# Performance work log

Measured on AMD Instinct MI355X. Metric: run time of the kernel, lower is better.

Reference implementation:

```python
import jax, jax.numpy as jnp
import numpy as np

D_MODEL = 768
D_HIDDEN = 2048
N_HEADS = 12
D_HEAD = 64
REG_COEFF = 1e-3
EPS = 1e-6
BATCH = 4
SEQ = 128


def setup_inputs() -> dict:
    key = jax.random.key(0)
    ks = jax.random.split(key, 4)
    # kaiming_uniform_ on (fan_in, fan_out)-shaped tensors: bound = sqrt(6 / fan_in_torch)
    # (values only need to be plausible; exact init dist is irrelevant for the kernel baseline)
    s_enc = 1.0 / np.sqrt(D_MODEL)
    s_dec = 1.0 / np.sqrt(D_HIDDEN)
    return {
        "x": jax.random.normal(ks[0], (BATCH, SEQ, D_MODEL), dtype=jnp.float32),
        "W_encQ": jax.random.normal(ks[1], (D_MODEL, D_HIDDEN), dtype=jnp.float32) * s_enc,
        "W_encK": jax.random.normal(ks[2], (D_MODEL, D_HIDDEN), dtype=jnp.float32) * s_enc,
        "b_encQ": jnp.zeros((D_HIDDEN,), dtype=jnp.float32),
        "b_encK": jnp.zeros((D_HIDDEN,), dtype=jnp.float32),
        "W_dec": jax.random.normal(ks[3], (D_HIDDEN, N_HEADS), dtype=jnp.float32) * s_dec,
        "b_dec": jnp.zeros((N_HEADS,), dtype=jnp.float32),
    }


def reference(x, W_encQ, W_encK, b_encQ, b_encK, W_dec, b_dec):
    # queries/keys: (batch, posn, d_hidden)
    queries = jax.nn.relu(jnp.einsum("bsd,dh->bsh", x, W_encQ) + b_encQ)
    keys = jax.nn.relu(jnp.einsum("bsd,dh->bsh", x, W_encK) + b_encK)
    # acts: (batch, posn_q, posn_k, d_hidden) -- the huge multi-use intermediate
    acts = queries[:, :, None, :] * keys[:, None, :, :]
    reg_loss = REG_COEFF * jnp.sum(jnp.sqrt(jnp.abs(acts) + EPS))
    feature_fires = (acts > 0).astype(jnp.int32)
    # decode to per-head scores: (batch, posn_q, posn_k, n_heads)
    score = jnp.einsum("bqkh,hn->bqkn", acts, W_dec) / np.sqrt(D_HEAD) + b_dec
    score = jnp.transpose(score, (0, 3, 1, 2))  # (batch, n_heads, posn_q, posn_k)
    return score, reg_loss, feature_fires
```

## Files before the change

### kernel.cpp

```cpp
#include <hip/hip_runtime.h>
#include <hip/hip_bf16.h>

#define D_MODEL 768
#define D_HIDDEN 2048
#define NHEADS 12
#define BATCH 4
#define SEQ 128
#define MROWS (BATCH*SEQ)
#define SCORE_ELEMS (BATCH*NHEADS*SEQ*SEQ)
#define REG_OFF SCORE_ELEMS
#define FIRES_OFF (SCORE_ELEMS + 1)
#define NROWS_T 65536
#define FIRES_WAVES 2048
#define FIRES_BLOCKS 512
#define SCORE_BLOCKS (BATCH*NHEADS*16)
#define TRIGCAP 64

typedef __attribute__((ext_vector_type(8))) short bf16x8;
typedef __attribute__((ext_vector_type(4))) float f32x4;

static __device__ __forceinline__ unsigned short f2bf(float f) {
    union { float f; unsigned u; } v; v.f = f;
    unsigned u = v.u;
    return (unsigned short)((u + 0x7FFFu + ((u >> 16) & 1u)) >> 16);
}

static __device__ __forceinline__ void split_bf16(float v, short& hi, short& lo) {
    unsigned short h = f2bf(v);
    float hf = __uint_as_float((unsigned)h << 16);
    float lf = v - hf;
    hi = (short)h;
    lo = (short)f2bf(lf);
}

static __device__ __forceinline__ float fsqrt_fast(float x) {
    return __builtin_amdgcn_sqrtf(x);
}

__global__ __launch_bounds__(256) void enc_kernel(
    const float* __restrict__ x,
    const float* __restrict__ WQ, const float* __restrict__ WK,
    const float* __restrict__ bQ, const float* __restrict__ bK,
    float* __restrict__ qbuf, float* __restrict__ kbuf,
    float* __restrict__ out)
{
    __shared__ unsigned tcnt;
    __shared__ unsigned tlist[TRIGCAP];
    __shared__ double   redd[4];

    const int bufid = blockIdx.z;
    const float* W    = bufid ? WK : WQ;
    const float* bias = bufid ? bK : bQ;
    float* outbuf     = bufid ? kbuf : qbuf;

    const int t  = threadIdx.x;
    if (t == 0) tcnt = 0u;
    if (blockIdx.x == 0 && blockIdx.y == 0 && blockIdx.z == 0 && t == 0)
        out[REG_OFF] = 0.f;
    __syncthreads();

    const int w  = t >> 6;
    const int l  = t & 63;
    const int mt = blockIdx.y * 64 + (w >> 1) * 32;
    const int nt = blockIdx.x * 64 + (w & 1) * 32;
    const int lr = l & 15;
    const int hg = (l >> 4) * 8;

    f32x4 acc[2][2];
    #pragma unroll
    for (int i = 0; i < 2; ++i)
        #pragma unroll
        for (int j = 0; j < 2; ++j) { f32x4 z = {0.f, 0.f, 0.f, 0.f}; acc[i][j] = z; }

    for (int kk = 0; kk < D_MODEL; kk += 32) {
        const int h0 = kk + hg;
        bf16x8 ah[2], al[2], bh[2], bl[2];
        #pragma unroll
        for (int fi = 0; fi < 2; ++fi) {
            const float* xp = x + (size_t)(mt + fi * 16 + lr) * D_MODEL + h0;
            const float4 v1 = *reinterpret_cast<const float4*>(xp);
            const float4 v2 = *reinterpret_cast<const float4*>(xp + 4);
            const float vv[8] = {v1.x, v1.y, v1.z, v1.w, v2.x, v2.y, v2.z, v2.w};
            #pragma unroll
            for (int i = 0; i < 8; ++i) {
                short h_, lo_;
                split_bf16(vv[i], h_, lo_);
                ah[fi][i] = h_; al[fi][i] = lo_;
            }
        }
        #pragma unroll
        for (int fj = 0; fj < 2; ++fj) {
            const int col = nt + fj * 16 + lr;
            #pragma unroll
            for (int i = 0; i < 8; ++i) {
                short h_, lo_;
                split_bf16(W[(size_t)(h0 + i) * D_HIDDEN + col], h_, lo_);
                bh[fj][i] = h_; bl[fj][i] = lo_;
            }
        }
        #pragma unroll
        for (int fi = 0; fi < 2; ++fi)
            #pragma unroll
            for (int fj = 0; fj < 2; ++fj) {
                acc[fi][fj] = __builtin_amdgcn_mfma_f32_16x16x32_bf16(
                    ah[fi], bh[fj], acc[fi][fj], 0, 0, 0);
                acc[fi][fj] = __builtin_amdgcn_mfma_f32_16x16x32_bf16(
                    ah[fi], bl[fj], acc[fi][fj], 0, 0, 0);
                acc[fi][fj] = __builtin_amdgcn_mfma_f32_16x16x32_bf16(
                    al[fi], bh[fj], acc[fi][fj], 0, 0, 0);
            }
    }

    #pragma unroll
    for (int fi = 0; fi < 2; ++fi)
        #pragma unroll
        for (int fj = 0; fj < 2; ++fj)
            #pragma unroll
            for (int j = 0; j < 4; ++j) {
                const int row = mt + fi * 16 + (l >> 4) * 4 + j;
                const int col = nt + fj * 16 + lr;
                float pre = acc[fi][fj][j] + bias[col];
                if (fabsf(pre) < 3e-4f) {
                    unsigned idx = atomicAdd(&tcnt, 1u);
                    if (idx < TRIGCAP) {
                        tlist[idx] = ((unsigned)row << 11) | (unsigned)col;
                    } else {
                        const float* xr = x + (size_t)row * D_MODEL;
                        const float* wc = W + col;
                        double s = (double)bias[col];
                        for (int dd = 0; dd < D_MODEL; ++dd)
                            s += (double)xr[dd] * (double)wc[(size_t)dd * D_HIDDEN];
                        pre = (float)s;
                    }
                }
                outbuf[(size_t)row * D_HIDDEN + col] = fmaxf(pre, 0.f);
            }

    __syncthreads();
    const unsigned n = min(tcnt, (unsigned)TRIGCAP);
    for (unsigned i = 0; i < n; ++i) {
        const unsigned e = tlist[i];
        const int hh = (int)(e & 2047u);
        const int mm = (int)(e >> 11);
        double s = 0.0;
        #pragma unroll
        for (int k = 0; k < 3; ++k) {
            const int dd = t + k * 256;
            s += (double)x[(size_t)mm * D_MODEL + dd]
               * (double)W[(size_t)dd * D_HIDDEN + hh];
        }
        #pragma unroll
        for (int off = 32; off > 0; off >>= 1) s += __shfl_down(s, off);
        if (l == 0) redd[w] = s;
        __syncthreads();
        if (t == 0) {
            double tot = redd[0] + redd[1] + redd[2] + redd[3] + (double)bias[hh];
            outbuf[(size_t)mm * D_HIDDEN + hh] = fmaxf((float)tot, 0.f);
        }
        __syncthreads();
    }
}

__global__ __launch_bounds__(256) void main_kernel(
    const float* __restrict__ qbuf, const float* __restrict__ kbuf,
    const float* __restrict__ Wdec, const float* __restrict__ bdec,
    float* __restrict__ out)
{
    __shared__ float wcol[D_HIDDEN];
    __shared__ float red[4][64][16];
    __shared__ float rs[4];
    const int t  = threadIdx.x;
    const int bi = blockIdx.x;

    if (bi < SCORE_BLOCKS) {
        const int sub = bi & 15;
        const int pr  = bi >> 4;
        const int n   = pr % NHEADS;
        const int b   = pr / NHEADS;

        for (int idx = t; idx < D_HIDDEN; idx += 256)
            wcol[idx] = Wdec[(size_t)idx * NHEADS + n];
        __syncthreads();

        const int qt   = (sub >> 2) * 32;
        const int kt   = (sub & 3) * 32;
        const int w    = t >> 6;
        const int lane = t & 63;
        const int lrow = lane & 15;
        const int koff = (lane >> 4) * 8;

        f32x4 acc[2][2];
        #pragma unroll
        for (int i = 0; i < 2; ++i)
            #pragma unroll
            for (int j = 0; j < 2; ++j) { f32x4 z = {0.f, 0.f, 0.f, 0.f}; acc[i][j] = z; }

        const float* qb = qbuf + (size_t)b * SEQ * D_HIDDEN;
        const float* kb = kbuf + (size_t)b * SEQ * D_HIDDEN;

        const int hlo = w * 512;
        for (int kk = hlo; kk < hlo + 512; kk += 32) {
            const int h0 = kk + koff;
            float wv[8];
            #pragma unroll
            for (int i = 0; i < 8; ++i) wv[i] = wcol[h0 + i];

            bf16x8 afrag[2], bfrag[2];
            #pragma unroll
            for (int fi = 0; fi < 2; ++fi) {
                const float* qp = qb + (size_t)(qt + fi * 16 + lrow) * D_HIDDEN + h0;
                const float4 q1 = *reinterpret_cast<const float4*>(qp);
                const float4 q2 = *reinterpret_cast<const float4*>(qp + 4);
                const float qf[8] = {q1.x, q1.y, q1.z, q1.w, q2.x, q2.y, q2.z, q2.w};
                #pragma unroll
                for (int i = 0; i < 8; ++i) afrag[fi][i] = (short)f2bf(qf[i] * wv[i]);
            }
            #pragma unroll
            for (int fj = 0; fj < 2; ++fj) {
                const float* kp = kb + (size_t)(kt + fj * 16 + lrow) * D_HIDDEN + h0;
                const float4 k1 = *reinterpret_cast<const float4*>(kp);
                const float4 k2 = *reinterpret_cast<const float4*>(kp + 4);
                const float kf[8] = {k1.x, k1.y, k1.z, k1.w, k2.x, k2.y, k2.z, k2.w};
                #pragma unroll
                for (int i = 0; i < 8; ++i) bfrag[fj][i] = (short)f2bf(kf[i]);
            }
            #pragma unroll
            for (int fi = 0; fi < 2; ++fi)
                #pragma unroll
                for (int fj = 0; fj < 2; ++fj)
                    acc[fi][fj] = __builtin_amdgcn_mfma_f32_16x16x32_bf16(
                        afrag[fi], bfrag[fj], acc[fi][fj], 0, 0, 0);
        }

        #pragma unroll
        for (int fi = 0; fi < 2; ++fi)
            #pragma unroll
            for (int fj = 0; fj < 2; ++fj)
                #pragma unroll
                for (int j = 0; j < 4; ++j)
                    red[w][lane][fi * 8 + fj * 4 + j] = acc[fi][fj][j];
        __syncthreads();

        const float bd   = bdec[n];
        const int   outb = (b * NHEADS + n) * SEQ * SEQ;
        #pragma unroll
        for (int u = 0; u < 4; ++u) {
            const int j = w * 4 + u;
            const float s = (red[0][lane][j] + red[1][lane][j])
                          + (red[2][lane][j] + red[3][lane][j]);
            const int fi = j >> 3, fj = (j >> 2) & 1, jj = j & 3;
            const int row = qt + fi * 16 + (lane >> 4) * 4 + jj;
            const int col = kt + fj * 16 + (lane & 15);
            out[outb + row * SEQ + col] = s * 0.125f + bd;
        }
        return;
    }

    const int w  = t >> 6;
    const int l  = t & 63;
    const int g  = (bi - SCORE_BLOCKS) * 4 + w;
    const int g7 = g >> 7;
    const int gk = g & 127;

    f32x4* out4 = reinterpret_cast<f32x4*>(out + FIRES_OFF - 1);
    float racc = 0.f;

    #pragma unroll 1
    for (int b = 0; b < 4; ++b) {
        const float* kr = kbuf + ((size_t)(b * SEQ) + gk) * D_HIDDEN;
        f32x4 kv[8];
        #pragma unroll
        for (int j = 0; j < 8; ++j)
            kv[j] = *reinterpret_cast<const f32x4*>(kr + 256 * j + 4 * l);
        float k3[8], k63[8];
        #pragma unroll
        for (int j = 0; j < 8; ++j) {
            k3[j]  = __shfl_up(kv[j][3], 1);
            k63[j] = __shfl(kv[j][3], 63);
        }

        #pragma unroll 1
        for (int ss = 0; ss < 8; ++ss) {
            const int s    = b * 8 + ss;
            const int R    = g + s * FIRES_WAVES;
            const int brow = s * 16 + g7;
            const float* qr = qbuf + (size_t)brow * D_HIDDEN;

            f32x4 qv[8];
            #pragma unroll
            for (int j = 0; j < 8; ++j)
                qv[j] = *reinterpret_cast<const f32x4*>(qr + 256 * j + 4 * l);

            float pm1 = 0.f;
            if (l == 0 && R > 0) {
                const int pbrow = (R - 1) >> 7;
                const int pb    = pbrow >> 7;
                const int pkrow = (pb << 7) + ((R - 1) & 127);
                pm1 = qbuf[(size_t)pbrow * D_HIDDEN + 2047]
                    * kbuf[(size_t)pkrow * D_HIDDEN + 2047];
            }

            float q3[8], q63[8];
            #pragma unroll
            for (int j = 0; j < 8; ++j) {
                q3[j]  = __shfl_up(qv[j][3], 1);
                q63[j] = __shfl(qv[j][3], 63);
            }

            #pragma unroll
            for (int j = 0; j < 8; ++j) {
                float p0;
                if (l == 0) {
                    p0 = (j == 0) ? pm1 : q63[j - 1] * k63[j - 1];
                } else {
                    p0 = q3[j] * k3[j];
                }
                const float p1 = qv[j][0] * kv[j][0];
                const float p2 = qv[j][1] * kv[j][1];
                const float p3 = qv[j][2] * kv[j][2];
                f32x4 f;
                f[0] = (p0 > 0.f) ? 1.f : 0.f;
                f[1] = (p1 > 0.f) ? 1.f : 0.f;
                f[2] = (p2 > 0.f) ? 1.f : 0.f;
                f[3] = (p3 > 0.f) ? 1.f : 0.f;
                if (R == 0 && j == 0 && l == 0) {
                    out[FIRES_OFF + 0] = f[1];
                    out[FIRES_OFF + 1] = f[2];
                    out[FIRES_OFF + 2] = f[3];
                } else {
                    out4[(size_t)R * 512 + 64 * j + l] = f;
                }
                racc += (fsqrt_fast(p0 + 1e-6f) + fsqrt_fast(p1 + 1e-6f))
                      + (fsqrt_fast(p2 + 1e-6f) + fsqrt_fast(p3 + 1e-6f));
            }
        }
    }

    if (g == 0 && l == 0) racc -= fsqrt_fast(1e-6f);
    if (g == FIRES_WAVES - 1 && l == 0) {
        const float pv = qbuf[(size_t)511 * D_HIDDEN + 2047]
                       * kbuf[(size_t)511 * D_HIDDEN + 2047];
        out[(size_t)(FIRES_OFF - 1) + (size_t)NROWS_T * D_HIDDEN] = (pv > 0.f) ? 1.f : 0.f;
        racc += fsqrt_fast(pv + 1e-6f);
    }

    #pragma unroll
    for (int off = 32; off > 0; off >>= 1) racc += __shfl_down(racc, off);
    if (l == 0) rs[w] = racc;
    __syncthreads();
    if (t == 0)
        atomicAdd(out + REG_OFF, ((rs[0] + rs[1]) + (rs[2] + rs[3])) * 1e-3f);
}

extern "C" void kernel_launch(void* const* d_in, const int* in_sizes, int n_in,
                              void* d_out, int out_size, void* d_ws, size_t ws_size,
                              hipStream_t stream) {
    const float* x  = (const float*)d_in[0];
    const float* WQ = (const float*)d_in[1];
    const float* WK = (const float*)d_in[2];
    const float* bQ = (const float*)d_in[3];
    const float* bK = (const float*)d_in[4];
    const float* Wd = (const float*)d_in[5];
    const float* bd = (const float*)d_in[6];
    float* out  = (float*)d_out;
    float* qbuf = (float*)d_ws;
    float* kbuf = qbuf + (size_t)MROWS * D_HIDDEN;

    dim3 b256(256);

    enc_kernel<<<dim3(D_HIDDEN / 64, MROWS / 64, 2), b256, 0, stream>>>(
        x, WQ, WK, bQ, bK, qbuf, kbuf, out);

    main_kernel<<<dim3(SCORE_BLOCKS + FIRES_BLOCKS), b256, 0, stream>>>(
        qbuf, kbuf, Wd, bd, out);
}
```

Measured before the change: 185.7 us.

## Precompute positivity bitmasks and split fires, score and reg-loss work into separate blocks

Adds a mask kernel that packs the sign of each query and key hidden value into 32-bit bitmasks. The fires path then writes its 0/1 outputs by ANDing the masks, so it no longer reloads float rows or multiplies them. The reg-loss sum moves into its own 512 blocks, each streaming key rows against one query row. Fires blocks are now scheduled first, ahead of the score blocks. This adds an extra kernel launch and a separate pass that rereads the key buffer, in exchange for lighter store-bound fires blocks.

```diff
diff --git a/kernel.cpp b/kernel.cpp
--- a/kernel.cpp
+++ b/kernel.cpp
@@ -14,6 +14,7 @@
 #define FIRES_WAVES 2048
 #define FIRES_BLOCKS 512
 #define SCORE_BLOCKS (BATCH*NHEADS*16)
+#define REG_BLOCKS 512
 #define TRIGCAP 64
 
 typedef __attribute__((ext_vector_type(8))) short bf16x8;
@@ -161,8 +162,29 @@
     }
 }
 
+__global__ __launch_bounds__(128) void mask_kernel(
+    const float* __restrict__ qbuf, const float* __restrict__ kbuf,
+    unsigned* __restrict__ qmask, unsigned* __restrict__ kmask)
+{
+    const int r = blockIdx.x;
+    const int t = threadIdx.x;
+    const int l = t & 63;
+    const float* src = (t < 64) ? qbuf : kbuf;
+    unsigned* dst    = (t < 64) ? qmask : kmask;
+    unsigned m = 0;
+    #pragma unroll
+    for (int j = 0; j < 8; ++j)
+        #pragma unroll
+        for (int e = 0; e < 4; ++e) {
+            const float v = src[(size_t)r * D_HIDDEN + 256 * j + 4 * l + e];
+            m |= (v > 0.f ? 1u : 0u) << (4 * j + e);
+        }
+    dst[r * 64 + l] = m;
+}
+
 __global__ __launch_bounds__(256) void main_kernel(
     const float* __restrict__ qbuf, const float* __restrict__ kbuf,
+    const unsigned* __restrict__ qmask, const unsigned* __restrict__ kmask,
     const float* __restrict__ Wdec, const float* __restrict__ bdec,
     float* __restrict__ out)
 {
@@ -171,10 +193,72 @@
     __shared__ float rs[4];
     const int t  = threadIdx.x;
     const int bi = blockIdx.x;
-
-    if (bi < SCORE_BLOCKS) {
-        const int sub = bi & 15;
-        const int pr  = bi >> 4;
+    const int w  = t >> 6;
+    const int l  = t & 63;
+
+    if (bi < FIRES_BLOCKS) {
+        const int g  = bi * 4 + w;
+        const int g7 = g >> 7;
+        const int gk = g & 127;
+
+        f32x4* out4 = reinterpret_cast<f32x4*>(out + FIRES_OFF - 1);
+
+        #pragma unroll 1
+        for (int b = 0; b < 4; ++b) {
+            const unsigned km = kmask[(b * SEQ + gk) * 64 + l];
+
+            #pragma unroll 1
+            for (int ss = 0; ss < 8; ++ss) {
+                const int s    = b * 8 + ss;
+                const int R    = g + s * FIRES_WAVES;
+                const int brow = s * 16 + g7;
+                const unsigned qm = qmask[brow * 64 + l];
+                const unsigned m   = qm & km;
+                const unsigned mp  = __shfl_up(m, 1);
+                const unsigned m63 = __shfl(m, 63);
+
+                unsigned pb1 = 0;
+                if (l == 0 && R > 0) {
+                    const int pbrow = (R - 1) >> 7;
+                    const int pb    = pbrow >> 7;
+                    const int pkrow = (pb << 7) + ((R - 1) & 127);
+                    pb1 = (qmask[pbrow * 64 + 63] >> 31)
+                        & (kmask[pkrow * 64 + 63] >> 31) & 1u;
+                }
+
+                #pragma unroll
+                for (int j = 0; j < 8; ++j) {
+                    unsigned b0;
+                    if (l == 0) b0 = (j == 0) ? pb1 : (m63 >> (4 * (j - 1) + 3)) & 1u;
+                    else        b0 = (mp >> (4 * j + 3)) & 1u;
+                    f32x4 f;
+                    f[0] = b0 ? 1.f : 0.f;
+                    f[1] = ((m >> (4 * j + 0)) & 1u) ? 1.f : 0.f;
+                    f[2] = ((m >> (4 * j + 1)) & 1u) ? 1.f : 0.f;
+                    f[3] = ((m >> (4 * j + 2)) & 1u) ? 1.f : 0.f;
+                    if (R == 0 && j == 0 && l == 0) {
+                        out[FIRES_OFF + 0] = f[1];
+                        out[FIRES_OFF + 1] = f[2];
+                        out[FIRES_OFF + 2] = f[3];
+                    } else {
+                        out4[(size_t)R * 512 + 64 * j + l] = f;
+                    }
+                }
+            }
+        }
+
+        if (bi == FIRES_BLOCKS - 1 && w == 3 && l == 0) {
+            const float pv = qbuf[(size_t)511 * D_HIDDEN + 2047]
+                           * kbuf[(size_t)511 * D_HIDDEN + 2047];
+            out[(size_t)(FIRES_OFF - 1) + (size_t)NROWS_T * D_HIDDEN] = (pv > 0.f) ? 1.f : 0.f;
+        }
+        return;
+    }
+
+    if (bi < FIRES_BLOCKS + SCORE_BLOCKS) {
+        const int sb  = bi - FIRES_BLOCKS;
+        const int sub = sb & 15;
+        const int pr  = sb >> 4;
         const int n   = pr % NHEADS;
         const int b   = pr / NHEADS;
 
@@ -184,10 +268,8 @@
 
         const int qt   = (sub >> 2) * 32;
         const int kt   = (sub & 3) * 32;
-        const int w    = t >> 6;
-        const int lane = t & 63;
-        const int lrow = lane & 15;
-        const int koff = (lane >> 4) * 8;
+        const int lrow = l & 15;
+        const int koff = (l >> 4) * 8;
 
         f32x4 acc[2][2];
         #pragma unroll
@@ -238,7 +320,7 @@
             for (int fj = 0; fj < 2; ++fj)
                 #pragma unroll
                 for (int j = 0; j < 4; ++j)
-                    red[w][lane][fi * 8 + fj * 4 + j] = acc[fi][fj][j];
+                    red[w][l][fi * 8 + fj * 4 + j] = acc[fi][fj][j];
         __syncthreads();
 
         const float bd   = bdec[n];
@@ -246,110 +328,44 @@
         #pragma unroll
         for (int u = 0; u < 4; ++u) {
             const int j = w * 4 + u;
-            const float s = (red[0][lane][j] + red[1][lane][j])
-                          + (red[2][lane][j] + red[3][lane][j]);
+            const float s = (red[0][l][j] + red[1][l][j])
+                          + (red[2][l][j] + red[3][l][j]);
             const int fi = j >> 3, fj = (j >> 2) & 1, jj = j & 3;
-            const int row = qt + fi * 16 + (lane >> 4) * 4 + jj;
-            const int col = kt + fj * 16 + (lane & 15);
+            const int row = qt + fi * 16 + (l >> 4) * 4 + jj;
+            const int col = kt + fj * 16 + (l & 15);
             out[outb + row * SEQ + col] = s * 0.125f + bd;
         }
         return;
     }
 
-    const int w  = t >> 6;
-    const int l  = t & 63;
-    const int g  = (bi - SCORE_BLOCKS) * 4 + w;
-    const int g7 = g >> 7;
-    const int gk = g & 127;
-
-    f32x4* out4 = reinterpret_cast<f32x4*>(out + FIRES_OFF - 1);
-    float racc = 0.f;
-
-    #pragma unroll 1
-    for (int b = 0; b < 4; ++b) {
-        const float* kr = kbuf + ((size_t)(b * SEQ) + gk) * D_HIDDEN;
-        f32x4 kv[8];
-        #pragma unroll
-        for (int j = 0; j < 8; ++j)
-            kv[j] = *reinterpret_cast<const f32x4*>(kr + 256 * j + 4 * l);
-        float k3[8], k63[8];
-        #pragma unroll
-        for (int j = 0; j < 8; ++j) {
-            k3[j]  = __shfl_up(kv[j][3], 1);
-            k63[j] = __shfl(kv[j][3], 63);
-        }
-
+    {
+        const int qr = bi - FIRES_BLOCKS - SCORE_BLOCKS;
+        const int b  = qr >> 7;
+        const float* qrow = qbuf + (size_t)qr * D_HIDDEN + t * 8;
+        const f32x4 q1 = *reinterpret_cast<const f32x4*>(qrow);
+        const f32x4 q2 = *reinterpret_cast<const f32x4*>(qrow + 4);
+
+        float acc = 0.f;
         #pragma unroll 1
-        for (int ss = 0; ss < 8; ++ss) {
-            const int s    = b * 8 + ss;
-            const int R    = g + s * FIRES_WAVES;
-            const int brow = s * 16 + g7;
-            const float* qr = qbuf + (size_t)brow * D_HIDDEN;
-
-            f32x4 qv[8];
-            #pragma unroll
-            for (int j = 0; j < 8; ++j)
-                qv[j] = *reinterpret_cast<const f32x4*>(qr + 256 * j + 4 * l);
-
-            float pm1 = 0.f;
-            if (l == 0 && R > 0) {
-                const int pbrow = (R - 1) >> 7;
-                const int pb    = pbrow >> 7;
-                const int pkrow = (pb << 7) + ((R - 1) & 127);
-                pm1 = qbuf[(size_t)pbrow * D_HIDDEN + 2047]
-                    * kbuf[(size_t)pkrow * D_HIDDEN + 2047];
-            }
-
-            float q3[8], q63[8];
-            #pragma unroll
-            for (int j = 0; j < 8; ++j) {
-                q3[j]  = __shfl_up(qv[j][3], 1);
-                q63[j] = __shfl(qv[j][3], 63);
-            }
-
-            #pragma unroll
-            for (int j = 0; j < 8; ++j) {
-                float p0;
-                if (l == 0) {
-                    p0 = (j == 0) ? pm1 : q63[j - 1] * k63[j - 1];
-                } else {
-                    p0 = q3[j] * k3[j];
-                }
-                const float p1 = qv[j][0] * kv[j][0];
-                const float p2 = qv[j][1] * kv[j][1];
-                const float p3 = qv[j][2] * kv[j][2];
-                f32x4 f;
-                f[0] = (p0 > 0.f) ? 1.f : 0.f;
-                f[1] = (p1 > 0.f) ? 1.f : 0.f;
-                f[2] = (p2 > 0.f) ? 1.f : 0.f;
-                f[3] = (p3 > 0.f) ? 1.f : 0.f;
-                if (R == 0 && j == 0 && l == 0) {
-                    out[FIRES_OFF + 0] = f[1];
-                    out[FIRES_OFF + 1] = f[2];
-                    out[FIRES_OFF + 2] = f[3];
-                } else {
-                    out4[(size_t)R * 512 + 64 * j + l] = f;
-                }
-                racc += (fsqrt_fast(p0 + 1e-6f) + fsqrt_fast(p1 + 1e-6f))
-                      + (fsqrt_fast(p2 + 1e-6f) + fsqrt_fast(p3 + 1e-6f));
-            }
-        }
-    }
-
-    if (g == 0 && l == 0) racc -= fsqrt_fast(1e-6f);
-    if (g == FIRES_WAVES - 1 && l == 0) {
-        const float pv = qbuf[(size_t)511 * D_HIDDEN + 2047]
-                       * kbuf[(size_t)511 * D_HIDDEN + 2047];
-        out[(size_t)(FIRES_OFF - 1) + (size_t)NROWS_T * D_HIDDEN] = (pv > 0.f) ? 1.f : 0.f;
-        racc += fsqrt_fast(pv + 1e-6f);
-    }
-
-    #pragma unroll
-    for (int off = 32; off > 0; off >>= 1) racc += __shfl_down(racc, off);
-    if (l == 0) rs[w] = racc;
-    __syncthreads();
-    if (t == 0)
-        atomicAdd(out + REG_OFF, ((rs[0] + rs[1]) + (rs[2] + rs[3])) * 1e-3f);
+        for (int k = 0; k < SEQ; ++k) {
+            const float* kp = kbuf + (size_t)(b * SEQ + k) * D_HIDDEN + t * 8;
+            const f32x4 k1 = *reinterpret_cast<const f32x4*>(kp);
+            const f32x4 k2 = *reinterpret_cast<const f32x4*>(kp + 4);
+            float s = 0.f;
+            #pragma unroll
+            for (int e = 0; e < 4; ++e) s += fsqrt_fast(q1[e] * k1[e] + 1e-6f);
+            #pragma unroll
+            for (int e = 0; e < 4; ++e) s += fsqrt_fast(q2[e] * k2[e] + 1e-6f);
+            acc += s;
+        }
+
+        #pragma unroll
+        for (int off = 32; off > 0; off >>= 1) acc += __shfl_down(acc, off);
+        if (l == 0) rs[w] = acc;
+        __syncthreads();
+        if (t == 0)
+            atomicAdd(out + REG_OFF, ((rs[0] + rs[1]) + (rs[2] + rs[3])) * 1e-3f);
+    }
 }
 
 extern "C" void kernel_launch(void* const* d_in, const int* in_sizes, int n_in,
@@ -365,12 +381,16 @@
     float* out  = (float*)d_out;
     float* qbuf = (float*)d_ws;
     float* kbuf = qbuf + (size_t)MROWS * D_HIDDEN;
+    unsigned* qmask = (unsigned*)(kbuf + (size_t)MROWS * D_HIDDEN);
+    unsigned* kmask = qmask + (size_t)MROWS * 64;
 
     dim3 b256(256);
 
     enc_kernel<<<dim3(D_HIDDEN / 64, MROWS / 64, 2), b256, 0, stream>>>(
         x, WQ, WK, bQ, bK, qbuf, kbuf, out);
 
-    main_kernel<<<dim3(SCORE_BLOCKS + FIRES_BLOCKS), b256, 0, stream>>>(
-        qbuf, kbuf, Wd, bd, out);
-}
+    mask_kernel<<<dim3(MROWS), dim3(128), 0, stream>>>(qbuf, kbuf, qmask, kmask);
+
+    main_kernel<<<dim3(FIRES_BLOCKS + SCORE_BLOCKS + REG_BLOCKS), b256, 0, stream>>>(
+        qbuf, kbuf, qmask, kmask, Wd, bd, out);
+}
```

New measurement: 196.8 us. +6.0%, slower.
